# Optimization experiments

Hardware: AMD Instinct MI355X
Metric: run time of the kernel (lower is better)

## Reference

```python
import jax, jax.numpy as jnp
import numpy as np

EPS = 1e-8
H_OUT, W_OUT = 64, 64
SURR_SCALE = 10.0  # SuperSpike-style surrogate slope

@jax.custom_vjp
def spike(x):
    # forward: Heaviside threshold
    return (x > 0).astype(x.dtype)

def _spike_fwd(x):
    return spike(x), x

def _spike_bwd(x, g):
    # SuperSpike surrogate gradient: 1/(1+scale*|x|)^2
    return (g / (1.0 + SURR_SCALE * jnp.abs(x)) ** 2,)

spike.defvjp(_spike_fwd, _spike_bwd)


def setup_inputs() -> dict:
    key = jax.random.key(0)
    k1, k2, k3, k4 = jax.random.split(key, 4)
    x = jax.random.normal(k1, (4, 16, 32, 64, 64), dtype=jnp.float32)
    # w ~ N(0, std*sqrt(1/(C_in*prod(kernel)))) with std=1
    w = jax.random.normal(k2, (64, 16, 3, 3, 3), dtype=jnp.float32) * np.float32(np.sqrt(1.0 / (16 * 27)))
    beta = jnp.clip(0.7 + 0.01 * jax.random.normal(k3, (1,), dtype=jnp.float32), 0.0, 1.0)
    b = jnp.clip(1.0 + 0.01 * jax.random.normal(k4, (64,), dtype=jnp.float32), 0.0, None)
    return {"x": x, "w": w, "beta": beta, "b": b}


def reference(x, w, beta, b):
    # x: (B, C_in, T, H, W); w: (C_out, C_in, kt, kh, kw)
    # conv3d, padding = ceil((k-1)*dil/2) = 1 per dim for k=3, dil=1
    conv_x = jax.lax.conv_general_dilated(
        x, w,
        window_strides=(1, 1, 1),
        padding=[(1, 1), (1, 1), (1, 1)],
        rhs_dilation=(1, 1, 1),
        dimension_numbers=("NCDHW", "OIDHW", "NCDHW"),
    )
    conv_x = conv_x[:, :, :, :H_OUT, :W_OUT]  # crop spatial dims only

    d = jnp.einsum("abcde,fbcde->af", w, w)          # (C_out, C_out) lateral matrix
    norm = jnp.sum(w ** 2, axis=(1, 2, 3, 4))        # (C_out,)
    inv_norm = 1.0 / (norm + EPS)
    beta_s = beta[0]

    B = x.shape[0]
    C = w.shape[0]
    mem0 = jnp.zeros((B, C, H_OUT, W_OUT), dtype=x.dtype)
    spk0 = jnp.zeros_like(mem0)

    xs = jnp.moveaxis(conv_x, 2, 0)  # (T, B, C, H, W)

    def step(carry, inp_t):
        spk, mem = carry
        rst = jnp.einsum("abcd,be->aecd", spk, d)  # lateral reset
        mem = (mem - rst) * beta_s + inp_t * (1.0 - beta_s)
        mthr = mem * inv_norm[None, :, None, None] - b[None, :, None, None]
        spk = spike(mthr)
        return (spk, mem), spk

    _, spk_rec = jax.lax.scan(step, (spk0, mem0), xs)  # (T, B, C, H, W)
    return jnp.moveaxis(spk_rec, 0, 2)  # (B, C, T, H, W) -- flatten_output=False
```

## Files before the change

kernel.cpp:

```cpp
#include <hip/hip_runtime.h>
#include <cstdint>
#include <cstddef>

#define H_ 64
#define W_ 64
#define T_ 32
#define CIN_ 16
#define COUT_ 64
#define K_ 432
#define TH_ 4
#define TW_ 16
#define WR_ 6
#define WC_ 24
#define WSZ_ (WR_ * WC_)
#define XTOT_ (CIN_ * WSZ_)
#define NSLOT_ 4
#define NTHR_ 512

__global__ void prep(const float* __restrict__ w, float* __restrict__ w_g,
                     double* __restrict__ d64, double* __restrict__ inv64) {
    const int i = blockIdx.x;
    const int j = threadIdx.x;
    const float* wi = w + i * K_;
    const float* wj = w + j * K_;
    double acc = 0.0;
    for (int k = 0; k < K_; ++k) acc += (double)wi[k] * (double)wj[k];
    d64[i * 64 + j] = acc;
    if (i == j) inv64[i] = 1.0 / (acc + 1e-8);
    for (int k = j; k < K_; k += 64)
        w_g[(((i >> 3) * K_) + k) * 8 + (i & 7)] = wi[k];
}

__launch_bounds__(NTHR_, 1)
__global__ void fused_snn(const float* __restrict__ xg,
                          const float* __restrict__ beta_g, const float* __restrict__ bias_g,
                          const float* __restrict__ w_g, const double* __restrict__ d64,
                          const double* __restrict__ inv64, float* __restrict__ out) {
    __shared__ __align__(16) float x_win[NSLOT_ * XTOT_];
    __shared__ __align__(16) double d_lds[64 * 65];
    __shared__ unsigned int masks[2][64][2];

    const int tid = threadIdx.x;
    const int b   = blockIdx.x;
    const int ty0 = blockIdx.y * TH_;
    const int tx0 = blockIdx.z * TW_;

    const int wv   = __builtin_amdgcn_readfirstlane(tid >> 6);
    const int lane = tid & 63;
    const int py   = lane >> 4;
    const int px   = lane & 15;
    const int c0   = wv * 8;
    const int xoff = py * WC_ + px;

    const float* wbase = w_g + (size_t)wv * (K_ * 8);

    for (int i = tid; i < 4096; i += NTHR_)
        d_lds[(i >> 6) * 65 + (i & 63)] = d64[i];
    if (tid < 128) masks[1][tid >> 1][tid & 1] = 0u;

    for (int z = 0; z < 2; ++z) {
        for (int i = tid; i < XTOT_; i += NTHR_) {
            int cin = i / WSZ_;
            int r2  = i - cin * WSZ_;
            int yy  = r2 / WC_;
            int xx  = r2 - yy * WC_;
            if (xx >= TW_ + 2) continue;
            int gy = ty0 - 1 + yy, gx = tx0 - 1 + xx;
            float v = 0.f;
            if (gy >= 0 && gy < H_ && gx >= 0 && gx < W_)
                v = xg[((size_t)(b * CIN_ + cin) * T_ + z) * (H_ * W_) + gy * W_ + gx];
            x_win[z * XTOT_ + i] = v;
        }
    }

    const double beta = (double)beta_g[0];
    const double omb  = 1.0 - beta;
    double inv_[8], bb[8];
#pragma unroll
    for (int ci = 0; ci < 8; ++ci) {
        inv_[ci] = inv64[c0 + ci];
        bb[ci]   = (double)bias_g[c0 + ci];
    }
    double mem[8];
#pragma unroll
    for (int ci = 0; ci < 8; ++ci) mem[ci] = 0.0;

    int  pf_loff[5];
    size_t pf_goff[5];
    bool pf_use[5], pf_in[5];
#pragma unroll
    for (int r = 0; r < 5; ++r) {
        int i = tid + r * NTHR_;
        int cin = i / WSZ_;
        int r2  = i - cin * WSZ_;
        int yy  = r2 / WC_;
        int xx  = r2 - yy * WC_;
        pf_loff[r] = i;
        int gy = ty0 - 1 + yy, gx = tx0 - 1 + xx;
        bool ok = (i < XTOT_) && (xx < TW_ + 2);
        pf_use[r] = ok;
        pf_in[r]  = ok && gy >= 0 && gy < H_ && gx >= 0 && gx < W_;
        pf_goff[r] = (size_t)(b * CIN_ + cin) * (T_ * H_ * W_) + (size_t)gy * W_ + gx;
    }

    for (int t = 0; t < T_; ++t) {
        __syncthreads();
        if (tid < 128) masks[t & 1][tid >> 1][tid & 1] = 0u;

        float R[5];
        const int zp = t + 2;
        if (zp < T_) {
#pragma unroll
            for (int r = 0; r < 5; ++r) {
                R[r] = 0.f;
                if (pf_in[r]) R[r] = xg[pf_goff[r] + (size_t)zp * (H_ * W_)];
            }
        }

        double accd[8];
#pragma unroll
        for (int ci = 0; ci < 8; ++ci) accd[ci] = 0.0;

        int slot_[3]; bool zok[3];
#pragma unroll
        for (int dz = 0; dz < 3; ++dz) {
            int z = t - 1 + dz;
            zok[dz]  = (z >= 0 && z < T_);
            slot_[dz] = zok[dz] ? (z & 3) : 0;
        }

        for (int cin = 0; cin < CIN_; ++cin) {
            float xv[3][9];
#pragma unroll
            for (int dz = 0; dz < 3; ++dz) {
                if (!zok[dz]) continue;
                const float* xs = &x_win[slot_[dz] * XTOT_ + cin * WSZ_] + xoff;
#pragma unroll
                for (int dy = 0; dy < 3; ++dy) {
                    xv[dz][dy * 3 + 0] = xs[dy * WC_ + 0];
                    xv[dz][dy * 3 + 1] = xs[dy * WC_ + 1];
                    xv[dz][dy * 3 + 2] = xs[dy * WC_ + 2];
                }
            }
            float cacc[8];
#pragma unroll
            for (int ci = 0; ci < 8; ++ci) cacc[ci] = 0.f;
#pragma unroll
            for (int dz = 0; dz < 3; ++dz) {
                if (!zok[dz]) continue;
                const float* wp = wbase + (cin * 27 + dz * 9) * 8;
#pragma unroll
                for (int dy = 0; dy < 3; ++dy) {
#pragma unroll
                    for (int j = 0; j < 3; ++j) {
                        const float xq = xv[dz][dy * 3 + j];
                        const float4 wa = *reinterpret_cast<const float4*>(wp + (dy * 3 + j) * 8);
                        const float4 wb = *reinterpret_cast<const float4*>(wp + (dy * 3 + j) * 8 + 4);
                        cacc[0] = fmaf(wa.x, xq, cacc[0]);
                        cacc[1] = fmaf(wa.y, xq, cacc[1]);
                        cacc[2] = fmaf(wa.z, xq, cacc[2]);
                        cacc[3] = fmaf(wa.w, xq, cacc[3]);
                        cacc[4] = fmaf(wb.x, xq, cacc[4]);
                        cacc[5] = fmaf(wb.y, xq, cacc[5]);
                        cacc[6] = fmaf(wb.z, xq, cacc[6]);
                        cacc[7] = fmaf(wb.w, xq, cacc[7]);
                    }
                }
            }
#pragma unroll
            for (int ci = 0; ci < 8; ++ci) accd[ci] += (double)cacc[ci];
        }

        double rstv[8];
#pragma unroll
        for (int ci = 0; ci < 8; ++ci) rstv[ci] = 0.0;
        const int rb = (t + 1) & 1;
#pragma unroll
        for (int wrd = 0; wrd < 2; ++wrd) {
            unsigned int m = masks[rb][lane][wrd];
            while (m) {
                int bit = __ffs(m) - 1;
                m &= m - 1;
                const double* drow = &d_lds[(wrd * 32 + bit) * 65 + c0];
#pragma unroll
                for (int ci = 0; ci < 8; ++ci) rstv[ci] += drow[ci];
            }
        }

        unsigned int nib = 0u;
        const size_t obase = ((size_t)(b * COUT_ + c0) * T_ + t) * (size_t)(H_ * W_)
                           + (size_t)(ty0 + py) * W_ + (tx0 + px);
#pragma unroll
        for (int ci = 0; ci < 8; ++ci) {
            mem[ci] = (mem[ci] - rstv[ci]) * beta + accd[ci] * omb;
            const double mthr = mem[ci] * inv_[ci] - bb[ci];
            const int s = mthr > 0.0 ? 1 : 0;
            out[obase + (size_t)ci * (T_ * H_ * W_)] = (float)s;
            nib |= (unsigned int)s << ci;
        }

        __syncthreads();
        if (nib) atomicOr(&masks[t & 1][lane][wv >> 2], nib << ((wv & 3) * 8));

        if (zp < T_) {
            const int so = (zp & 3) * XTOT_;
#pragma unroll
            for (int r = 0; r < 5; ++r)
                if (pf_use[r]) x_win[so + pf_loff[r]] = R[r];
        }
    }
}

extern "C" void kernel_launch(void* const* d_in, const int* in_sizes, int n_in,
                              void* d_out, int out_size, void* d_ws, size_t ws_size,
                              hipStream_t stream) {
    const float* x    = (const float*)d_in[0];
    const float* w    = (const float*)d_in[1];
    const float* beta = (const float*)d_in[2];
    const float* bias = (const float*)d_in[3];
    float* out = (float*)d_out;

    float*  w_g   = (float*)d_ws;
    double* d64   = (double*)((char*)d_ws + 110592);
    double* inv64 = (double*)((char*)d_ws + 110592 + 32768);

    prep<<<dim3(64), dim3(64), 0, stream>>>(w, w_g, d64, inv64);
    fused_snn<<<dim3(4, 16, 4), dim3(NTHR_), 0, stream>>>(x, beta, bias, w_g, d64, inv64, out);
}
```

Baseline: 526.2 us.

## Load conv inputs directly from global memory with register double-buffering

Drops the shared-memory sliding window of input time slices and its per-step prefetch and store. Each thread now reads its 27-point neighbourhood straight from global memory through clamped addresses and zero masks, relying on the cache for reuse. Loads are double-buffered in registers across pairs of input channels to overlap load latency with FMAs. This removes LDS traffic and the cooperative staging, but each of the 8 waves redundantly issues global/L1 loads for the same input values and register pressure rises.

```diff
diff --git a/kernel.cpp b/kernel.cpp
--- a/kernel.cpp
+++ b/kernel.cpp
@@ -8,13 +8,6 @@
 #define CIN_ 16
 #define COUT_ 64
 #define K_ 432
-#define TH_ 4
-#define TW_ 16
-#define WR_ 6
-#define WC_ 24
-#define WSZ_ (WR_ * WC_)
-#define XTOT_ (CIN_ * WSZ_)
-#define NSLOT_ 4
 #define NTHR_ 512
 
 __global__ void prep(const float* __restrict__ w, float* __restrict__ w_g,
@@ -31,26 +24,57 @@
         w_g[(((i >> 3) * K_) + k) * 8 + (i & 7)] = wi[k];
 }
 
+#define LOADX(CIN, XV) do {                                                      \
+    const float* xm_ = xg + (((size_t)(b * 16 + (CIN)) * 32 + zmc) << 12);       \
+    const float* x0_ = xg + (((size_t)(b * 16 + (CIN)) * 32 + t  ) << 12);       \
+    const float* xp_ = xg + (((size_t)(b * 16 + (CIN)) * 32 + zpc) << 12);       \
+    _Pragma("unroll")                                                            \
+    for (int j_ = 0; j_ < 9; ++j_) {                                             \
+        XV[j_]      = xm_[a9[j_]] * mA[j_];                                      \
+        XV[9 + j_]  = x0_[a9[j_]] * m9[j_];                                      \
+        XV[18 + j_] = xp_[a9[j_]] * mC[j_];                                      \
+    }                                                                            \
+} while (0)
+
+#define FMACIN(CIN, XV) do {                                                     \
+    float cacc[8] = {0.f, 0.f, 0.f, 0.f, 0.f, 0.f, 0.f, 0.f};                    \
+    const float* wp_ = wbase + (CIN) * 216;               \
+    _Pragma("unroll")                                                            \
+    for (int k_ = 0; k_ < 27; ++k_) {                                            \
+        const float xq = XV[k_];                                                 \
+        const float4 wa = *reinterpret_cast<const float4*>(wp_ + k_ * 8);        \
+        const float4 wb = *reinterpret_cast<const float4*>(wp_ + k_ * 8 + 4);    \
+        cacc[0] = fmaf(wa.x, xq, cacc[0]);                                       \
+        cacc[1] = fmaf(wa.y, xq, cacc[1]);                                       \
+        cacc[2] = fmaf(wa.z, xq, cacc[2]);                                       \
+        cacc[3] = fmaf(wa.w, xq, cacc[3]);                                       \
+        cacc[4] = fmaf(wb.x, xq, cacc[4]);                                       \
+        cacc[5] = fmaf(wb.y, xq, cacc[5]);                                       \
+        cacc[6] = fmaf(wb.z, xq, cacc[6]);                                       \
+        cacc[7] = fmaf(wb.w, xq, cacc[7]);                                       \
+    }                                                                            \
+    _Pragma("unroll")                                                            \
+    for (int ci_ = 0; ci_ < 8; ++ci_) accd[ci_] += (double)cacc[ci_];            \
+} while (0)
+
 __launch_bounds__(NTHR_, 1)
 __global__ void fused_snn(const float* __restrict__ xg,
                           const float* __restrict__ beta_g, const float* __restrict__ bias_g,
                           const float* __restrict__ w_g, const double* __restrict__ d64,
                           const double* __restrict__ inv64, float* __restrict__ out) {
-    __shared__ __align__(16) float x_win[NSLOT_ * XTOT_];
     __shared__ __align__(16) double d_lds[64 * 65];
     __shared__ unsigned int masks[2][64][2];
 
     const int tid = threadIdx.x;
     const int b   = blockIdx.x;
-    const int ty0 = blockIdx.y * TH_;
-    const int tx0 = blockIdx.z * TW_;
+    const int ty0 = blockIdx.y * 4;
+    const int tx0 = blockIdx.z * 16;
 
     const int wv   = __builtin_amdgcn_readfirstlane(tid >> 6);
     const int lane = tid & 63;
     const int py   = lane >> 4;
     const int px   = lane & 15;
     const int c0   = wv * 8;
-    const int xoff = py * WC_ + px;
 
     const float* wbase = w_g + (size_t)wv * (K_ * 8);
 
@@ -58,20 +82,19 @@
         d_lds[(i >> 6) * 65 + (i & 63)] = d64[i];
     if (tid < 128) masks[1][tid >> 1][tid & 1] = 0u;
 
-    for (int z = 0; z < 2; ++z) {
-        for (int i = tid; i < XTOT_; i += NTHR_) {
-            int cin = i / WSZ_;
-            int r2  = i - cin * WSZ_;
-            int yy  = r2 / WC_;
-            int xx  = r2 - yy * WC_;
-            if (xx >= TW_ + 2) continue;
-            int gy = ty0 - 1 + yy, gx = tx0 - 1 + xx;
-            float v = 0.f;
-            if (gy >= 0 && gy < H_ && gx >= 0 && gx < W_)
-                v = xg[((size_t)(b * CIN_ + cin) * T_ + z) * (H_ * W_) + gy * W_ + gx];
-            x_win[z * XTOT_ + i] = v;
+    int a9[9];
+    float m9[9];
+    const int gy0 = ty0 + py - 1, gx0 = tx0 + px - 1;
+#pragma unroll
+    for (int dy = 0; dy < 3; ++dy)
+#pragma unroll
+        for (int dx = 0; dx < 3; ++dx) {
+            const int gy = gy0 + dy, gx = gx0 + dx;
+            const int cy = gy < 0 ? 0 : (gy > 63 ? 63 : gy);
+            const int cx = gx < 0 ? 0 : (gx > 63 ? 63 : gx);
+            a9[dy * 3 + dx] = cy * 64 + cx;
+            m9[dy * 3 + dx] = (gy >= 0 && gy < 64 && gx >= 0 && gx < 64) ? 1.f : 0.f;
         }
-    }
 
     const double beta = (double)beta_g[0];
     const double omb  = 1.0 - beta;
@@ -85,90 +108,34 @@
 #pragma unroll
     for (int ci = 0; ci < 8; ++ci) mem[ci] = 0.0;
 
-    int  pf_loff[5];
-    size_t pf_goff[5];
-    bool pf_use[5], pf_in[5];
-#pragma unroll
-    for (int r = 0; r < 5; ++r) {
-        int i = tid + r * NTHR_;
-        int cin = i / WSZ_;
-        int r2  = i - cin * WSZ_;
-        int yy  = r2 / WC_;
-        int xx  = r2 - yy * WC_;
-        pf_loff[r] = i;
-        int gy = ty0 - 1 + yy, gx = tx0 - 1 + xx;
-        bool ok = (i < XTOT_) && (xx < TW_ + 2);
-        pf_use[r] = ok;
-        pf_in[r]  = ok && gy >= 0 && gy < H_ && gx >= 0 && gx < W_;
-        pf_goff[r] = (size_t)(b * CIN_ + cin) * (T_ * H_ * W_) + (size_t)gy * W_ + gx;
-    }
+    __syncthreads();
 
     for (int t = 0; t < T_; ++t) {
         __syncthreads();
         if (tid < 128) masks[t & 1][tid >> 1][tid & 1] = 0u;
 
-        float R[5];
-        const int zp = t + 2;
-        if (zp < T_) {
+        const int zmc = t > 0 ? t - 1 : 0;
+        const int zpc = t < 31 ? t + 1 : 31;
+        const float fA = t > 0 ? 1.f : 0.f;
+        const float fC = t < 31 ? 1.f : 0.f;
+        float mA[9], mC[9];
 #pragma unroll
-            for (int r = 0; r < 5; ++r) {
-                R[r] = 0.f;
-                if (pf_in[r]) R[r] = xg[pf_goff[r] + (size_t)zp * (H_ * W_)];
-            }
-        }
+        for (int j = 0; j < 9; ++j) { mA[j] = m9[j] * fA; mC[j] = m9[j] * fC; }
 
         double accd[8];
 #pragma unroll
         for (int ci = 0; ci < 8; ++ci) accd[ci] = 0.0;
 
-        int slot_[3]; bool zok[3];
-#pragma unroll
-        for (int dz = 0; dz < 3; ++dz) {
-            int z = t - 1 + dz;
-            zok[dz]  = (z >= 0 && z < T_);
-            slot_[dz] = zok[dz] ? (z & 3) : 0;
-        }
-
-        for (int cin = 0; cin < CIN_; ++cin) {
-            float xv[3][9];
-#pragma unroll
-            for (int dz = 0; dz < 3; ++dz) {
-                if (!zok[dz]) continue;
-                const float* xs = &x_win[slot_[dz] * XTOT_ + cin * WSZ_] + xoff;
-#pragma unroll
-                for (int dy = 0; dy < 3; ++dy) {
-                    xv[dz][dy * 3 + 0] = xs[dy * WC_ + 0];
-                    xv[dz][dy * 3 + 1] = xs[dy * WC_ + 1];
-                    xv[dz][dy * 3 + 2] = xs[dy * WC_ + 2];
-                }
+        {
+            float xvA[27], xvB[27];
+            LOADX(0, xvA);
+#pragma unroll 1
+            for (int g = 0; g < 8; ++g) {
+                LOADX(2 * g + 1, xvB);
+                FMACIN(2 * g, xvA);
+                if (g < 7) LOADX(2 * g + 2, xvA);
+                FMACIN(2 * g + 1, xvB);
             }
-            float cacc[8];
-#pragma unroll
-            for (int ci = 0; ci < 8; ++ci) cacc[ci] = 0.f;
-#pragma unroll
-            for (int dz = 0; dz < 3; ++dz) {
-                if (!zok[dz]) continue;
-                const float* wp = wbase + (cin * 27 + dz * 9) * 8;
-#pragma unroll
-                for (int dy = 0; dy < 3; ++dy) {
-#pragma unroll
-                    for (int j = 0; j < 3; ++j) {
-                        const float xq = xv[dz][dy * 3 + j];
-                        const float4 wa = *reinterpret_cast<const float4*>(wp + (dy * 3 + j) * 8);
-                        const float4 wb = *reinterpret_cast<const float4*>(wp + (dy * 3 + j) * 8 + 4);
-                        cacc[0] = fmaf(wa.x, xq, cacc[0]);
-                        cacc[1] = fmaf(wa.y, xq, cacc[1]);
-                        cacc[2] = fmaf(wa.z, xq, cacc[2]);
-                        cacc[3] = fmaf(wa.w, xq, cacc[3]);
-                        cacc[4] = fmaf(wb.x, xq, cacc[4]);
-                        cacc[5] = fmaf(wb.y, xq, cacc[5]);
-                        cacc[6] = fmaf(wb.z, xq, cacc[6]);
-                        cacc[7] = fmaf(wb.w, xq, cacc[7]);
-                    }
-                }
-            }
-#pragma unroll
-            for (int ci = 0; ci < 8; ++ci) accd[ci] += (double)cacc[ci];
         }
 
         double rstv[8];
@@ -201,13 +168,6 @@
 
         __syncthreads();
         if (nib) atomicOr(&masks[t & 1][lane][wv >> 2], nib << ((wv & 3) * 8));
-
-        if (zp < T_) {
-            const int so = (zp & 3) * XTOT_;
-#pragma unroll
-            for (int r = 0; r < 5; ++r)
-                if (pf_use[r]) x_win[so + pf_loff[r]] = R[r];
-        }
     }
 }
 
```

Result: slower. 1.426 ms (+171.1%).
